# Performance work log

Measured on AMD Instinct MI355X. Metric: run time of the kernel, lower is better.

Reference implementation:

```python
import jax, jax.numpy as jnp
import numpy as np

B, S, I, H = 128, 512, 256, 512

def setup_inputs() -> dict:
    key = jax.random.key(0)
    ks = jax.random.split(key, 8)
    s_wd = 1.0 / np.sqrt(H)
    s_u = 1.0 / np.sqrt(I)
    return {
        "inputs": jax.random.normal(ks[0], (B, S, I), dtype=jnp.float32),
        "timestamps": jax.random.uniform(ks[1], (B, S), dtype=jnp.float32),
        "W_all_w": jax.random.uniform(ks[2], (4 * H, H), minval=-s_wd, maxval=s_wd, dtype=jnp.float32),
        "W_all_b": jax.random.uniform(ks[3], (4 * H,), minval=-s_wd, maxval=s_wd, dtype=jnp.float32),
        "U_all_w": jax.random.uniform(ks[4], (4 * H, I), minval=-s_u, maxval=s_u, dtype=jnp.float32),
        "U_all_b": jax.random.uniform(ks[5], (4 * H,), minval=-s_u, maxval=s_u, dtype=jnp.float32),
        "W_d_w": jax.random.uniform(ks[6], (H, H), minval=-s_wd, maxval=s_wd, dtype=jnp.float32),
        "W_d_b": jax.random.uniform(ks[7], (H,), minval=-s_wd, maxval=s_wd, dtype=jnp.float32),
    }

def reference(inputs, timestamps, W_all_w, W_all_b, U_all_w, U_all_b, W_d_w, W_d_b):
    b, seq, _ = inputs.shape
    hdim = W_d_w.shape[0]
    # Precompute input projection for all steps: [b, s, 4H] -> scan over [s, b, 4H]
    u_all = jnp.einsum("bsi,gi->bsg", inputs, U_all_w) + U_all_b
    u_seq = jnp.swapaxes(u_all, 0, 1)          # [s, b, 4H]
    t_seq = jnp.swapaxes(timestamps, 0, 1)     # [s, b]

    def step(carry, xs):
        h, c = carry
        u, t = xs
        c_s1 = jnp.tanh(c @ W_d_w.T + W_d_b)
        c_adj = c - c_s1 + c_s1 * t[:, None]   # c_l + c_s2
        outs = h @ W_all_w.T + W_all_b + u
        f, i, o, c_tmp = jnp.split(outs, 4, axis=1)
        f = jax.nn.sigmoid(f)
        i = jax.nn.sigmoid(i)
        o = jax.nn.sigmoid(o)
        c_tmp = jax.nn.sigmoid(c_tmp)
        c_new = f * c_adj + i * c_tmp
        h_new = o * jnp.tanh(c_new)
        return (h_new, c_new), h_new

    h0 = jnp.zeros((b, hdim), dtype=inputs.dtype)
    c0 = jnp.zeros((b, hdim), dtype=inputs.dtype)
    _, outputs = jax.lax.scan(step, (h0, c0), (u_seq, t_seq))
    return jnp.swapaxes(outputs, 0, 1)         # [b, s, H]
```

## Files before the change

kernel.cpp:

```cpp
#include <hip/hip_runtime.h>


#define Bq 128
#define Sq 512
#define Iq 256
#define Hq 512

typedef __bf16  bf16x8  __attribute__((ext_vector_type(8)));
typedef float   floatx4 __attribute__((ext_vector_type(4)));
typedef unsigned short ushort;
typedef ushort  ushort8 __attribute__((ext_vector_type(8)));

__device__ __forceinline__ ushort f2bf(float f) {
    union { float f; unsigned u; } v; v.f = f;
    unsigned r = v.u + 0x7fffu + ((v.u >> 16) & 1u);
    return (ushort)(r >> 16);
}

__device__ __forceinline__ float sigm(float x) { return 1.f / (1.f + __expf(-x)); }
__device__ __forceinline__ float tanh_fast(float x) {
    float e = __expf(2.f * x);
    return 1.f - 2.f / (e + 1.f);
}

__device__ __forceinline__ void gl_lds16(const void* g, void* l) {
    __builtin_amdgcn_global_load_lds(
        (const __attribute__((address_space(1))) unsigned int*)g,
        (__attribute__((address_space(3))) unsigned int*)l, 16, 0, 0);
}

__device__ __forceinline__ bf16x8 pack8(float4 a, float4 b) {
    ushort8 v;
    v[0] = f2bf(a.x); v[1] = f2bf(a.y); v[2] = f2bf(a.z); v[3] = f2bf(a.w);
    v[4] = f2bf(b.x); v[5] = f2bf(b.y); v[6] = f2bf(b.z); v[7] = f2bf(b.w);
    return __builtin_bit_cast(bf16x8, v);
}

__global__ __launch_bounds__(256, 1) void lstm_kernel(
    const float* __restrict__ xin,
    const float* __restrict__ tsp,
    const float* __restrict__ Ww, const float* __restrict__ Wb,
    const float* __restrict__ Uw, const float* __restrict__ Ub,
    const float* __restrict__ Dw, const float* __restrict__ Db,
    unsigned* __restrict__ hcbuf,
    unsigned* __restrict__ slots,
    float* __restrict__ out)
{
    __shared__ ushort h_s[16 * 520];
    __shared__ ushort c_s[16 * 520];
    __shared__ ushort x_s[16 * 264];
    __shared__ float  x32_s[16 * 260];
    __shared__ float  gb[4 * 256];
    __shared__ float  gd[4 * 256];
    __shared__ float  bias_g[64];
    __shared__ float  bias_d[16];

    const int tid  = threadIdx.x;
    const int lane = tid & 63;
    const int wv   = tid >> 6;
    const int n    = lane & 15;
    const int quad = lane >> 4;
    const int gq   = blockIdx.x & 7;
    const int s    = blockIdx.x >> 3;
    const int jj   = s * 16;

    bf16x8 bW[16], bU[8], bD[4];
    {
        const int Rw = wv * Hq + jj + n;
        #pragma unroll
        for (int kk = 0; kk < 16; ++kk) {
            const float4* p = (const float4*)(Ww + (size_t)Rw * Hq + kk * 32 + quad * 8);
            bW[kk] = pack8(p[0], p[1]);
        }
        #pragma unroll
        for (int kk = 0; kk < 8; ++kk) {
            const float4* p = (const float4*)(Uw + (size_t)Rw * Iq + kk * 32 + quad * 8);
            bU[kk] = pack8(p[0], p[1]);
        }
        const int Rd = jj + n;
        #pragma unroll
        for (int kq = 0; kq < 4; ++kq) {
            const float4* p = (const float4*)(Dw + (size_t)Rd * Hq + (wv * 4 + kq) * 32 + quad * 8);
            bD[kq] = pack8(p[0], p[1]);
        }
    }
    if (tid < 64)
        bias_g[tid] = Wb[(tid >> 4) * Hq + jj + (tid & 15)] + Ub[(tid >> 4) * Hq + jj + (tid & 15)];
    if (tid >= 64 && tid < 80)
        bias_d[tid - 64] = Db[jj + (tid - 64)];
    __syncthreads();

    float c_reg = 0.f;
    const int b = tid >> 4, j = tid & 15;
    const int grow = gq * 16 + b;

    const ushort* hp = &h_s[n * 520 + quad * 8];
    const ushort* cp = &c_s[n * 520 + quad * 8];
    const ushort* xp = &x_s[n * 264 + quad * 8];

    unsigned* myslot = &slots[gq * 64 + s];
    unsigned* pollp  = &slots[gq * 64 + (lane & 31)];

    for (int t = 0; t < Sq; ++t) {
        float tt = tsp[(size_t)grow * Sq + t];

        #pragma unroll
        for (int q = 0; q < 4; ++q) {
            int r = q * 4 + wv;
            gl_lds16(xin + ((size_t)(gq * 16 + r) * Sq + t) * Iq + lane * 4, &x32_s[r * 260]);
        }

        unsigned* hcsrc = hcbuf + ((size_t)(t & 1) * 8 + gq) * 8192;
        unsigned v[32];
        #pragma unroll
        for (int q = 0; q < 32; ++q)
            v[q] = __hip_atomic_load(hcsrc + q * 256 + tid, __ATOMIC_RELAXED, __HIP_MEMORY_SCOPE_AGENT);

        #pragma unroll
        for (int q = 0; q < 32; ++q) {
            const int row = q >> 1, col = ((q & 1) << 8) + tid;
            h_s[row * 520 + col] = (ushort)(v[q] & 0xFFFFu);
            c_s[row * 520 + col] = (ushort)(v[q] >> 16);
        }
        __syncthreads();

        {
            const int rr = tid >> 4, seg = tid & 15;
            const float4* src = (const float4*)&x32_s[rr * 260 + seg * 16];
            float4 a0 = src[0], a1 = src[1], a2 = src[2], a3 = src[3];
            ushort8 v0, v1;
            v0[0] = f2bf(a0.x); v0[1] = f2bf(a0.y); v0[2] = f2bf(a0.z); v0[3] = f2bf(a0.w);
            v0[4] = f2bf(a1.x); v0[5] = f2bf(a1.y); v0[6] = f2bf(a1.z); v0[7] = f2bf(a1.w);
            v1[0] = f2bf(a2.x); v1[1] = f2bf(a2.y); v1[2] = f2bf(a2.z); v1[3] = f2bf(a2.w);
            v1[4] = f2bf(a3.x); v1[5] = f2bf(a3.y); v1[6] = f2bf(a3.z); v1[7] = f2bf(a3.w);
            *(ushort8*)&x_s[rr * 264 + seg * 16]     = v0;
            *(ushort8*)&x_s[rr * 264 + seg * 16 + 8] = v1;
        }
        __syncthreads();

        floatx4 accW = {0.f, 0.f, 0.f, 0.f};
        floatx4 accU = {0.f, 0.f, 0.f, 0.f};
        floatx4 accD = {0.f, 0.f, 0.f, 0.f};
        #pragma unroll
        for (int kk = 0; kk < 16; ++kk) {
            bf16x8 ah = *(const bf16x8*)(hp + kk * 32);
            accW = __builtin_amdgcn_mfma_f32_16x16x32_bf16(ah, bW[kk], accW, 0, 0, 0);
            if (kk < 8) {
                bf16x8 ax = *(const bf16x8*)(xp + kk * 32);
                accU = __builtin_amdgcn_mfma_f32_16x16x32_bf16(ax, bU[kk], accU, 0, 0, 0);
            }
            if ((kk >> 2) == wv) {
                bf16x8 ac = *(const bf16x8*)(cp + kk * 32);
                accD = __builtin_amdgcn_mfma_f32_16x16x32_bf16(ac, bD[kk & 3], accD, 0, 0, 0);
            }
        }
        accW += accU;

        #pragma unroll
        for (int r2 = 0; r2 < 4; ++r2) {
            gb[wv * 256 + (quad * 4 + r2) * 16 + n] = accW[r2];
            gd[wv * 256 + (quad * 4 + r2) * 16 + n] = accD[r2];
        }
        __syncthreads();

        float pf = gb[tid]       + bias_g[j];
        float pi = gb[256 + tid] + bias_g[16 + j];
        float po = gb[512 + tid] + bias_g[32 + j];
        float pc = gb[768 + tid] + bias_g[48 + j];
        float csum = gd[tid] + gd[256 + tid] + gd[512 + tid] + gd[768 + tid] + bias_d[j];
        float c_s1  = tanh_fast(csum);
        float c_adj = c_reg - c_s1 + c_s1 * tt;
        float fg = sigm(pf), ig = sigm(pi), og = sigm(po), cg = sigm(pc);
        float c_new = fg * c_adj + ig * cg;
        float h_new = og * tanh_fast(c_new);
        c_reg = c_new;

        out[((size_t)grow * Sq + t) * Hq + jj + j] = h_new;
        unsigned* hcdst = hcbuf + ((size_t)((t + 1) & 1) * 8 + gq) * 8192;
        unsigned hc = ((unsigned)f2bf(c_new) << 16) | (unsigned)f2bf(h_new);
        __hip_atomic_store(hcdst + b * 512 + jj + j, hc, __ATOMIC_RELAXED, __HIP_MEMORY_SCOPE_AGENT);
        __syncthreads();

        if (t < Sq - 1) {
            unsigned tgt = (unsigned)(t + 1);
            if (tid == 0)
                __hip_atomic_store(myslot, tgt, __ATOMIC_RELAXED, __HIP_MEMORY_SCOPE_AGENT);
            if (wv == 0) {
                for (;;) {
                    unsigned vv = __hip_atomic_load(pollp, __ATOMIC_RELAXED, __HIP_MEMORY_SCOPE_AGENT);
                    if (__all(vv >= tgt)) break;
                    __builtin_amdgcn_s_sleep(2);
                }
            }
            __syncthreads();
        }
    }
}

extern "C" void kernel_launch(void* const* d_in, const int* in_sizes, int n_in,
                              void* d_out, int out_size, void* d_ws, size_t ws_size,
                              hipStream_t stream) {
    const float* inputs = (const float*)d_in[0];
    const float* tsp    = (const float*)d_in[1];
    const float* Ww     = (const float*)d_in[2];
    const float* Wb     = (const float*)d_in[3];
    const float* Uw     = (const float*)d_in[4];
    const float* Ub     = (const float*)d_in[5];
    const float* Dw     = (const float*)d_in[6];
    const float* Db     = (const float*)d_in[7];
    float* out = (float*)d_out;

    char* ws = (char*)d_ws;
    unsigned* hcbuf = (unsigned*)ws;
    unsigned* slots = (unsigned*)(ws + 524288);

    hipMemsetAsync(ws, 0, 262144, stream);
    hipMemsetAsync(ws + 524288, 0, 2048, stream);

    lstm_kernel<<<dim3(256), dim3(256), 0, stream>>>(
        inputs, tsp, Ww, Wb, Uw, Ub, Dw, Db, hcbuf, slots, out);
}
```

Before: 2.226 ms.

## Use per-wave flags, split h/c buffers, and prefetch inputs in registers

Replaces the per-block barrier-and-slot handshake with one flag per wave. Every wave polls all flags in its group directly, which removes the trailing __syncthreads around the cross-block exchange. The interleaved h/c word buffer is split into separate h and c planes, packed two bf16 values per word via a lane shuffle, and read back with 64-bit loads. Next-step inputs are prefetched into registers during the wait instead of staged through LDS with global_load_lds. This shortens the critical path of each recurrent step, at the cost of more flag polling traffic and reliance on vmcnt waits for memory ordering.

```diff
diff --git a/kernel.cpp b/kernel.cpp
--- a/kernel.cpp
+++ b/kernel.cpp
@@ -10,6 +10,7 @@
 typedef float   floatx4 __attribute__((ext_vector_type(4)));
 typedef unsigned short ushort;
 typedef ushort  ushort8 __attribute__((ext_vector_type(8)));
+typedef unsigned long long u64;
 
 __device__ __forceinline__ ushort f2bf(float f) {
     union { float f; unsigned u; } v; v.f = f;
@@ -21,12 +22,6 @@
 __device__ __forceinline__ float tanh_fast(float x) {
     float e = __expf(2.f * x);
     return 1.f - 2.f / (e + 1.f);
-}
-
-__device__ __forceinline__ void gl_lds16(const void* g, void* l) {
-    __builtin_amdgcn_global_load_lds(
-        (const __attribute__((address_space(1))) unsigned int*)g,
-        (__attribute__((address_space(3))) unsigned int*)l, 16, 0, 0);
 }
 
 __device__ __forceinline__ bf16x8 pack8(float4 a, float4 b) {
@@ -49,7 +44,6 @@
     __shared__ ushort h_s[16 * 520];
     __shared__ ushort c_s[16 * 520];
     __shared__ ushort x_s[16 * 264];
-    __shared__ float  x32_s[16 * 260];
     __shared__ float  gb[4 * 256];
     __shared__ float  gd[4 * 256];
     __shared__ float  bias_g[64];
@@ -98,43 +92,46 @@
     const ushort* cp = &c_s[n * 520 + quad * 8];
     const ushort* xp = &x_s[n * 264 + quad * 8];
 
-    unsigned* myslot = &slots[gq * 64 + s];
-    unsigned* pollp  = &slots[gq * 64 + (lane & 31)];
+    unsigned* flagbase = slots + gq * 128;
+    unsigned* myflag   = flagbase + s * 4 + wv;
+    const unsigned* poll0 = flagbase + lane;
+    const unsigned* poll1 = flagbase + 64 + lane;
+
+    const float* xbase = xin + ((size_t)(gq * 16 + (tid >> 4)) * Sq) * Iq + (tid & 15) * 16;
+    float4 x0, x1, x2, x3;
+    {
+        const float4* p = (const float4*)xbase;
+        x0 = p[0]; x1 = p[1]; x2 = p[2]; x3 = p[3];
+    }
 
     for (int t = 0; t < Sq; ++t) {
         float tt = tsp[(size_t)grow * Sq + t];
 
-        #pragma unroll
-        for (int q = 0; q < 4; ++q) {
-            int r = q * 4 + wv;
-            gl_lds16(xin + ((size_t)(gq * 16 + r) * Sq + t) * Iq + lane * 4, &x32_s[r * 260]);
-        }
-
-        unsigned* hcsrc = hcbuf + ((size_t)(t & 1) * 8 + gq) * 8192;
-        unsigned v[32];
-        #pragma unroll
-        for (int q = 0; q < 32; ++q)
-            v[q] = __hip_atomic_load(hcsrc + q * 256 + tid, __ATOMIC_RELAXED, __HIP_MEMORY_SCOPE_AGENT);
-
-        #pragma unroll
-        for (int q = 0; q < 32; ++q) {
-            const int row = q >> 1, col = ((q & 1) << 8) + tid;
-            h_s[row * 520 + col] = (ushort)(v[q] & 0xFFFFu);
-            c_s[row * 520 + col] = (ushort)(v[q] >> 16);
-        }
-        __syncthreads();
+        const u64* hsrc = (const u64*)(hcbuf + ((size_t)(t & 1) * 8 + gq) * 8192);
+        const u64* csrc = hsrc + 2048;
+        u64 hv[8], cv[8];
+        #pragma unroll
+        for (int k = 0; k < 8; ++k)
+            hv[k] = __hip_atomic_load(hsrc + k * 256 + tid, __ATOMIC_RELAXED, __HIP_MEMORY_SCOPE_AGENT);
+        #pragma unroll
+        for (int k = 0; k < 8; ++k)
+            cv[k] = __hip_atomic_load(csrc + k * 256 + tid, __ATOMIC_RELAXED, __HIP_MEMORY_SCOPE_AGENT);
 
         {
-            const int rr = tid >> 4, seg = tid & 15;
-            const float4* src = (const float4*)&x32_s[rr * 260 + seg * 16];
-            float4 a0 = src[0], a1 = src[1], a2 = src[2], a3 = src[3];
-            ushort8 v0, v1;
-            v0[0] = f2bf(a0.x); v0[1] = f2bf(a0.y); v0[2] = f2bf(a0.z); v0[3] = f2bf(a0.w);
-            v0[4] = f2bf(a1.x); v0[5] = f2bf(a1.y); v0[6] = f2bf(a1.z); v0[7] = f2bf(a1.w);
-            v1[0] = f2bf(a2.x); v1[1] = f2bf(a2.y); v1[2] = f2bf(a2.z); v1[3] = f2bf(a2.w);
-            v1[4] = f2bf(a3.x); v1[5] = f2bf(a3.y); v1[6] = f2bf(a3.z); v1[7] = f2bf(a3.w);
-            *(ushort8*)&x_s[rr * 264 + seg * 16]     = v0;
-            *(ushort8*)&x_s[rr * 264 + seg * 16 + 8] = v1;
+            bf16x8 v0 = pack8(x0, x1);
+            bf16x8 v1 = pack8(x2, x3);
+            ushort* xd = &x_s[(tid >> 4) * 264 + (tid & 15) * 16];
+            *(bf16x8*)xd       = v0;
+            *(bf16x8*)(xd + 8) = v1;
+        }
+
+        #pragma unroll
+        for (int k = 0; k < 8; ++k) {
+            const int m   = k * 256 + tid;
+            const int row = m >> 7;
+            const int col = (m << 2) & 511;
+            *(u64*)&h_s[row * 520 + col] = hv[k];
+            *(u64*)&c_s[row * 520 + col] = cv[k];
         }
         __syncthreads();
 
@@ -176,23 +173,39 @@
         c_reg = c_new;
 
         out[((size_t)grow * Sq + t) * Hq + jj + j] = h_new;
-        unsigned* hcdst = hcbuf + ((size_t)((t + 1) & 1) * 8 + gq) * 8192;
-        unsigned hc = ((unsigned)f2bf(c_new) << 16) | (unsigned)f2bf(h_new);
-        __hip_atomic_store(hcdst + b * 512 + jj + j, hc, __ATOMIC_RELAXED, __HIP_MEMORY_SCOPE_AGENT);
-        __syncthreads();
+
+        {
+            unsigned my    = ((unsigned)f2bf(c_new) << 16) | (unsigned)f2bf(h_new);
+            unsigned other = __shfl_xor(my, 1);
+            unsigned* dst  = hcbuf + ((size_t)((t + 1) & 1) * 8 + gq) * 8192;
+            const int pidx = b * 256 + ((jj + j) >> 1);
+            if ((j & 1) == 0) {
+                unsigned hpair = ((other & 0xFFFFu) << 16) | (my & 0xFFFFu);
+                __hip_atomic_store(dst + pidx, hpair, __ATOMIC_RELAXED, __HIP_MEMORY_SCOPE_AGENT);
+            } else {
+                unsigned cpair = (my & 0xFFFF0000u) | (other >> 16);
+                __hip_atomic_store(dst + 4096 + pidx, cpair, __ATOMIC_RELAXED, __HIP_MEMORY_SCOPE_AGENT);
+            }
+        }
 
         if (t < Sq - 1) {
-            unsigned tgt = (unsigned)(t + 1);
-            if (tid == 0)
-                __hip_atomic_store(myslot, tgt, __ATOMIC_RELAXED, __HIP_MEMORY_SCOPE_AGENT);
-            if (wv == 0) {
-                for (;;) {
-                    unsigned vv = __hip_atomic_load(pollp, __ATOMIC_RELAXED, __HIP_MEMORY_SCOPE_AGENT);
-                    if (__all(vv >= tgt)) break;
-                    __builtin_amdgcn_s_sleep(2);
-                }
-            }
-            __syncthreads();
+            asm volatile("s_waitcnt vmcnt(0)" ::: "memory");
+            const unsigned tgt = (unsigned)(t + 1);
+            if (lane == 0)
+                __hip_atomic_store(myflag, tgt, __ATOMIC_RELAXED, __HIP_MEMORY_SCOPE_AGENT);
+
+            {
+                const float4* p = (const float4*)(xbase + (size_t)(t + 1) * Iq);
+                x0 = p[0]; x1 = p[1]; x2 = p[2]; x3 = p[3];
+            }
+
+            for (;;) {
+                unsigned a0 = __hip_atomic_load(poll0, __ATOMIC_RELAXED, __HIP_MEMORY_SCOPE_AGENT);
+                unsigned a1 = __hip_atomic_load(poll1, __ATOMIC_RELAXED, __HIP_MEMORY_SCOPE_AGENT);
+                if (__all(a0 >= tgt && a1 >= tgt)) break;
+                __builtin_amdgcn_s_sleep(2);
+            }
+            asm volatile("" ::: "memory");
         }
     }
 }
@@ -215,7 +228,7 @@
     unsigned* slots = (unsigned*)(ws + 524288);
 
     hipMemsetAsync(ws, 0, 262144, stream);
-    hipMemsetAsync(ws + 524288, 0, 2048, stream);
+    hipMemsetAsync(ws + 524288, 0, 4096, stream);
 
     lstm_kernel<<<dim3(256), dim3(256), 0, stream>>>(
         inputs, tsp, Ww, Wb, Uw, Ub, Dw, Db, hcbuf, slots, out);
```

Result: slower. 4.744 ms (+113.1%).
